# Kernel tuning notes

Hardware: AMD Instinct MI355X
Metric: run time of the kernel (lower is better)

## Reference

```python
import jax, jax.numpy as jnp
import numpy as np

B, LD, LQ = 32, 512, 32
E, NF = 300, 4
D = E + NF            # doc_input_size = 304
M = 16                # fofe_max_length == max_len
ALPHA = 0.9
VOCAB = 50000
H = 256
SAMPLE_NUM = 256
POS_N = 128           # int(sample_num * (1 - neg_ratio))
NEG_N = SAMPLE_NUM - POS_N
R = min(M, LD - 2)    # candidate negative lengths = 16
PPL = NEG_N // R + 1  # negatives drawn per length = 9


def setup_inputs() -> dict:
    key = jax.random.key(0)
    ks = jax.random.split(key, 16)
    emb = jax.random.normal(ks[0], (VOCAB, E), jnp.float32) * 0.1
    emb = emb.at[0].set(0.0)  # padding_idx=0
    doc = jax.random.randint(ks[1], (B, LD), 1, VOCAB)
    doc_f = jax.random.normal(ks[2], (B, LD, NF), jnp.float32) * 0.1
    query = jax.random.randint(ks[3], (B, LQ), 1, VOCAB)
    target_s = jax.random.randint(ks[4], (B,), 1, LD - M - 2)
    span = jax.random.randint(ks[5], (B,), 0, M)  # ans_span = target_e - target_s < fofe_max_length
    target_e = target_s + span
    rand_length = jax.random.permutation(ks[6], R)  # torch.randperm(min(max_len, L-2))
    # rand_position[i] ~ randint(1, LD - rand_length[i] - 1)
    u = jax.random.uniform(ks[7], (R, PPL))
    size = (LD - rand_length - 2).astype(jnp.float32)[:, None]
    rand_position = 1 + jnp.floor(u * size).astype(jnp.int32)
    rand_idx = jax.random.randint(ks[8], (NEG_N,), 0, B)  # faithful to original (dim-0 size used as bound)
    perm_idx = jax.random.permutation(ks[9], SAMPLE_NUM)

    def w(k, o, i):
        return jax.random.normal(k, (o, i), jnp.float32) * (1.0 / np.sqrt(i))

    CIN = 3 * D + E  # 1212
    W1 = w(ks[10], 4 * H, CIN)
    W2 = w(ks[11], 4 * H, 4 * H)
    W3 = w(ks[12], 4 * H, 4 * H)
    W4 = w(ks[13], 2 * H, 4 * H)
    W5 = w(ks[14], 1, 2 * H)
    doc_mask = jnp.zeros((B, LD), bool)
    query_mask = jnp.zeros((B, LQ), bool)
    return dict(doc=doc, doc_f=doc_f, query=query, target_s=target_s, target_e=target_e,
                doc_mask=doc_mask, query_mask=query_mask, emb=emb,
                W1=W1, W2=W2, W3=W3, W4=W4, W5=W5,
                rand_length=rand_length, rand_position=rand_position,
                rand_idx=rand_idx, perm_idx=perm_idx)


def _fofe_codes(x):
    """x: [B, D, LD] -> forward/inverse FOFE codes [B, D, M, LD].
    fwd[b,c,l,t] = sum_{k=0}^{l} alpha^k x[b,c,t-k]; inv mirrors to the right."""
    fwd_terms = jnp.stack(
        [(ALPHA ** k) * jnp.pad(x, ((0, 0), (0, 0), (k, 0)))[..., :LD] for k in range(M)], axis=2)
    inv_terms = jnp.stack(
        [(ALPHA ** k) * jnp.pad(x, ((0, 0), (0, 0), (0, k)))[..., k:] for k in range(M)], axis=2)
    return jnp.cumsum(fwd_terms, axis=2), jnp.cumsum(inv_terms, axis=2)


def _cnn(x, W1, W2, W3, W4, W5):
    h = jax.nn.relu(jnp.einsum('oi,bis->bos', W1, x))
    h = jax.nn.relu(jnp.einsum('oi,bis->bos', W2, h))
    h = jax.nn.relu(jnp.einsum('oi,bis->bos', W3, h))
    h = jax.nn.relu(jnp.einsum('oi,bis->bos', W4, h))
    return jax.nn.sigmoid(jnp.einsum('oi,bis->bos', W5, h))


def reference(doc, doc_f, query, target_s, target_e, doc_mask, query_mask, emb,
              W1, W2, W3, W4, W5, rand_length, rand_position, rand_idx, perm_idx):
    # input_embedding (dropout_emb = 0, pos/ner disabled)
    doc_input = jnp.concatenate([emb[doc], doc_f], axis=-1)  # [B, LD, D]
    x = jnp.swapaxes(doc_input, 1, 2)                         # [B, D, LD]
    fwd, inv = _fofe_codes(x)                                 # [B, D, M, LD] each

    # --- positive samples: gold span + left/right full contexts ---
    b = jnp.arange(B)
    span = target_e - target_s
    ans = fwd[b, :, span, target_e]                               # [B, D]
    l_ctx = fwd[b, :, M - 1, jnp.maximum(target_s - 1, 0)]        # [B, D]
    r_ctx = inv[b, :, M - 1, jnp.minimum(target_e + 1, LD - 1)]   # [B, D]
    pos = jnp.concatenate([l_ctx, ans, r_ctx], axis=-1)          # [B, 3D]
    pos = jnp.broadcast_to(pos[:, :, None], (B, 3 * D, POS_N))

    # --- negative samples: random spans of each length in rand_length ---
    rl = rand_length[:, None]                                     # [R, 1]
    neg_ans = fwd[:, :, rl, rand_position].reshape(B, D, R * PPL)
    neg_l = fwd[:, :, M - 1, rand_position - 1].reshape(B, D, R * PPL)
    neg_r = inv[:, :, M - 1, rand_position + rl + 1].reshape(B, D, R * PPL)
    rand_cat = jnp.concatenate([neg_l, neg_ans, neg_r], axis=1)   # [B, 3D, R*PPL]
    neg = rand_cat[:, :, rand_idx]                                # [B, 3D, NEG_N]

    # --- shuffle pos+neg, build query FOFE, run cnn, mse (sum) loss ---
    ctx_ans = jnp.concatenate([pos, neg], axis=-1)[:, :, perm_idx]
    target = jnp.concatenate(
        [jnp.ones((B, 1, POS_N), jnp.float32), jnp.zeros((B, 1, NEG_N), jnp.float32)],
        axis=-1)[:, :, perm_idx]
    qw = ALPHA ** jnp.arange(LQ - 1, -1, -1, dtype=jnp.float32)   # fofe_linear weights
    qf = jnp.einsum('t,bte->be', qw, emb[query])                  # [B, E]
    qb = jnp.broadcast_to(qf[:, :, None], (B, E, SAMPLE_NUM))
    dq_input = jnp.concatenate([ctx_ans, qb], axis=1)             # [B, 3D+E, S]
    score = _cnn(dq_input, W1, W2, W3, W4, W5)                    # [B, 1, S]
    loss = jnp.sum((score - target) ** 2)                         # mse_loss(size_average=False)
    return loss
```

## Files before the change

### kernel.cpp

```cpp
#include <hip/hip_runtime.h>
#include <hip/hip_bf16.h>

#define B_    32
#define LD_   512
#define LQ_   32
#define E_    300
#define NF_   4
#define D_    304
#define M_    16
#define ALPHA_ 0.9f
#define CIN_  1212
#define KP1_  1216
#define NCOL_ 1056
#define NPAD_ 1088
#define PPL_  9
#define NEG_N_ 128

typedef short short8 __attribute__((ext_vector_type(8)));
typedef float f32x4 __attribute__((ext_vector_type(4)));

__device__ __forceinline__ unsigned short f2bf(float f) {
    unsigned int x = __float_as_uint(f);
    unsigned int r = (x + 0x7FFFu + ((x >> 16) & 1u)) >> 16;
    return (unsigned short)r;
}
__device__ __forceinline__ float bf2f(unsigned short u) {
    return __uint_as_float(((unsigned int)u) << 16);
}

__global__ __launch_bounds__(128) void query_fofe(
    const int* __restrict__ query, const float* __restrict__ emb,
    unsigned short* __restrict__ qfb)
{
    int b = blockIdx.x;
    __shared__ int   rows[32];
    __shared__ float wq[32];
    int tid = threadIdx.x;
    if (tid < 32) {
        rows[tid] = query[b * LQ_ + tid];
        wq[tid] = powf(ALPHA_, (float)(LQ_ - 1 - tid));
    }
    __syncthreads();
    if (tid < 76) {
        int cc = tid * 4;
        float ax = 0.f, ay = 0.f, az = 0.f, aw = 0.f;
        if (cc < 300) {
            for (int i = 0; i < 32; ++i) {
                float4 v = *(const float4*)(emb + (size_t)rows[i] * E_ + cc);
                float wv = wq[i];
                ax += wv * v.x; ay += wv * v.y; az += wv * v.z; aw += wv * v.w;
            }
        }
        ushort4 o; o.x = f2bf(ax); o.y = f2bf(ay); o.z = f2bf(az); o.w = f2bf(aw);
        *(ushort4*)(qfb + (size_t)b * 304 + cc) = o;
    }
}

__global__ __launch_bounds__(320) void build_features(
    const int* __restrict__ doc, const float* __restrict__ doc_f,
    const int* __restrict__ target_s, const int* __restrict__ target_e,
    const float* __restrict__ emb,
    const int* __restrict__ rand_length, const int* __restrict__ rand_position,
    const unsigned short* __restrict__ qfb,
    unsigned short* __restrict__ Ft)
{
    int bcol = blockIdx.x;
    int b = bcol / 33;
    int col = bcol % 33;
    __shared__ int   s_t[3][16];
    __shared__ float s_w[3][16];
    __shared__ int   s_row[3][16];
    int tid = threadIdx.x;

    if (tid < 48) {
        int part = tid >> 4, k = tid & 15;
        int t; float valid;
        if (col == 0) {
            int ts = target_s[b], te = target_e[b];
            int span = te - ts;
            if (part == 0)      { t = ts - 1 - k;  valid = (t >= 0) ? 1.f : 0.f; }
            else if (part == 1) { t = te - k;      valid = (k <= span && t >= 0) ? 1.f : 0.f; }
            else                { t = te + 1 + k;  valid = (t < LD_) ? 1.f : 0.f; }
        } else {
            int j = col - 1;
            int r = j / PPL_, p = j - r * PPL_;
            int rl = rand_length[r];
            int rp = rand_position[r * PPL_ + p];
            if (part == 0)      { t = rp - 1 - k;      valid = (t >= 0) ? 1.f : 0.f; }
            else if (part == 1) { t = rp - k;          valid = (k <= rl && t >= 0) ? 1.f : 0.f; }
            else                { t = rp + rl + 1 + k; valid = (t < LD_) ? 1.f : 0.f; }
        }
        float w = (valid != 0.f) ? powf(ALPHA_, (float)k) : 0.f;
        t = min(max(t, 0), LD_ - 1);
        s_t[part][k] = t;
        s_w[part][k] = w;
        s_row[part][k] = doc[b * LD_ + t];
    }
    __syncthreads();

    unsigned short* out = Ft + (size_t)bcol * KP1_;
    int g = tid;
    if (g < 228) {
        int part = g / 76;
        int g2 = g - part * 76;
        int cc = g2 * 4;
        float ax = 0.f, ay = 0.f, az = 0.f, aw = 0.f;
        if (cc < 300) {
            for (int i = 0; i < 16; ++i) {
                float4 v = *(const float4*)(emb + (size_t)s_row[part][i] * E_ + cc);
                float wv = s_w[part][i];
                ax += wv * v.x; ay += wv * v.y; az += wv * v.z; aw += wv * v.w;
            }
        } else {
            for (int i = 0; i < 16; ++i) {
                float4 v = *(const float4*)(doc_f + ((size_t)b * LD_ + s_t[part][i]) * NF_);
                float wv = s_w[part][i];
                ax += wv * v.x; ay += wv * v.y; az += wv * v.z; aw += wv * v.w;
            }
        }
        ushort4 o; o.x = f2bf(ax); o.y = f2bf(ay); o.z = f2bf(az); o.w = f2bf(aw);
        *(ushort4*)(out + 4 * g) = o;
    } else if (g < 303) {
        *(ushort4*)(out + 4 * g) =
            *(const ushort4*)(qfb + (size_t)b * 304 + (g - 228) * 4);
    } else if (g == 303) {
        ushort4 z; z.x = 0; z.y = 0; z.z = 0; z.w = 0;
        *(ushort4*)(out + 4 * g) = z;
    }
}

__global__ __launch_bounds__(256) void convert_all(
    const float* __restrict__ W1, const float* __restrict__ W2,
    const float* __restrict__ W3, const float* __restrict__ W4,
    unsigned short* __restrict__ W1b, unsigned short* __restrict__ W2b,
    unsigned short* __restrict__ W3b, unsigned short* __restrict__ W4b)
{
    const long n1 = 1024L * KP1_ / 4;
    const long n2 = 1024L * 1024L / 4;
    const long n4 = 512L * 1024L / 4;
    const long total = n1 + 2 * n2 + n4;
    long stride = (long)gridDim.x * 256L;
    for (long i = (long)blockIdx.x * 256L + threadIdx.x; i < total; i += stride) {
        ushort4 o;
        if (i < n1) {
            long m = i / 304; int k4 = (int)(i - m * 304);
            if (k4 < 303) {
                float4 v = *(const float4*)(W1 + m * CIN_ + k4 * 4);
                o.x = f2bf(v.x); o.y = f2bf(v.y); o.z = f2bf(v.z); o.w = f2bf(v.w);
            } else { o.x = 0; o.y = 0; o.z = 0; o.w = 0; }
            *(ushort4*)(W1b + i * 4) = o;
        } else if (i < n1 + n2) {
            long j = i - n1;
            float4 v = *(const float4*)(W2 + j * 4);
            o.x = f2bf(v.x); o.y = f2bf(v.y); o.z = f2bf(v.z); o.w = f2bf(v.w);
            *(ushort4*)(W2b + j * 4) = o;
        } else if (i < n1 + 2 * n2) {
            long j = i - n1 - n2;
            float4 v = *(const float4*)(W3 + j * 4);
            o.x = f2bf(v.x); o.y = f2bf(v.y); o.z = f2bf(v.z); o.w = f2bf(v.w);
            *(ushort4*)(W3b + j * 4) = o;
        } else {
            long j = i - n1 - 2 * n2;
            float4 v = *(const float4*)(W4 + j * 4);
            o.x = f2bf(v.x); o.y = f2bf(v.y); o.z = f2bf(v.z); o.w = f2bf(v.w);
            *(ushort4*)(W4b + j * 4) = o;
        }
    }
}

__global__ __launch_bounds__(256) void gemm_relu(
    const unsigned short* __restrict__ A,
    const unsigned short* __restrict__ Bm,
    unsigned short* __restrict__ C,
    int M, int K)
{
    __shared__ unsigned short As[2][64][72];
    __shared__ unsigned short Bs[2][64][72];
    int tid = threadIdx.x;
    int m0 = blockIdx.x * 64, n0 = blockIdx.y * 64;
    int w = tid >> 6, lane = tid & 63;
    int wm = (w >> 1) * 32, wn = (w & 1) * 32;
    int lr = tid >> 2;
    int ls = (tid & 3) * 16;
    int fr = lane & 15, fk = (lane >> 4) * 8;

    const unsigned short* Arow = A + (size_t)(m0 + lr) * K + ls;
    const unsigned short* Brow = Bm + (size_t)(n0 + lr) * K + ls;

    f32x4 acc00 = {0.f,0.f,0.f,0.f}, acc01 = {0.f,0.f,0.f,0.f};
    f32x4 acc10 = {0.f,0.f,0.f,0.f}, acc11 = {0.f,0.f,0.f,0.f};

    int nk = K >> 6;
    {
        uint4 a0 = *(const uint4*)(Arow);
        uint4 a1 = *(const uint4*)(Arow + 8);
        uint4 b0 = *(const uint4*)(Brow);
        uint4 b1 = *(const uint4*)(Brow + 8);
        *(uint4*)&As[0][lr][ls]     = a0;
        *(uint4*)&As[0][lr][ls + 8] = a1;
        *(uint4*)&Bs[0][lr][ls]     = b0;
        *(uint4*)&Bs[0][lr][ls + 8] = b1;
    }
    __syncthreads();
    int cur = 0;
    for (int i = 0; i < nk; ++i) {
        uint4 na0, na1, nb0, nb1;
        bool more = (i + 1 < nk);
        if (more) {
            const unsigned short* An = Arow + (size_t)(i + 1) * 64;
            const unsigned short* Bn = Brow + (size_t)(i + 1) * 64;
            na0 = *(const uint4*)(An);
            na1 = *(const uint4*)(An + 8);
            nb0 = *(const uint4*)(Bn);
            nb1 = *(const uint4*)(Bn + 8);
        }
        #pragma unroll
        for (int s = 0; s < 2; ++s) {
            short8 fa0 = *(const short8*)&As[cur][wm + fr][s * 32 + fk];
            short8 fa1 = *(const short8*)&As[cur][wm + 16 + fr][s * 32 + fk];
            short8 fb0 = *(const short8*)&Bs[cur][wn + fr][s * 32 + fk];
            short8 fb1 = *(const short8*)&Bs[cur][wn + 16 + fr][s * 32 + fk];
            acc00 = __builtin_amdgcn_mfma_f32_16x16x32_bf16(fa0, fb0, acc00, 0, 0, 0);
            acc01 = __builtin_amdgcn_mfma_f32_16x16x32_bf16(fa0, fb1, acc01, 0, 0, 0);
            acc10 = __builtin_amdgcn_mfma_f32_16x16x32_bf16(fa1, fb0, acc10, 0, 0, 0);
            acc11 = __builtin_amdgcn_mfma_f32_16x16x32_bf16(fa1, fb1, acc11, 0, 0, 0);
        }
        if (more) {
            int nb = cur ^ 1;
            *(uint4*)&As[nb][lr][ls]     = na0;
            *(uint4*)&As[nb][lr][ls + 8] = na1;
            *(uint4*)&Bs[nb][lr][ls]     = nb0;
            *(uint4*)&Bs[nb][lr][ls + 8] = nb1;
        }
        __syncthreads();
        cur ^= 1;
    }

    int rbase = (lane >> 4) * 4;
    int cb = lane & 15;
    #define STORE_TILE(ACC, MT, NT) do {                                   \
        int m = m0 + wm + (MT) * 16 + rbase;                               \
        int n = n0 + wn + (NT) * 16 + cb;                                  \
        ushort4 o;                                                         \
        o.x = f2bf(fmaxf((ACC)[0], 0.f));                                  \
        o.y = f2bf(fmaxf((ACC)[1], 0.f));                                  \
        o.z = f2bf(fmaxf((ACC)[2], 0.f));                                  \
        o.w = f2bf(fmaxf((ACC)[3], 0.f));                                  \
        *(ushort4*)(C + (size_t)n * M + m) = o;                            \
    } while (0)
    STORE_TILE(acc00, 0, 0);
    STORE_TILE(acc01, 0, 1);
    STORE_TILE(acc10, 1, 0);
    STORE_TILE(acc11, 1, 1);
    #undef STORE_TILE
}

__global__ __launch_bounds__(256) void score_loss(
    const unsigned short* __restrict__ h4,
    const float* __restrict__ W5, const int* __restrict__ rand_idx,
    float* __restrict__ out)
{
    __shared__ int cnt[32];
    __shared__ float part[4];
    int tid = threadIdx.x;
    if (tid < 32) cnt[tid] = 0;
    __syncthreads();
    if (tid < NEG_N_) atomicAdd(&cnt[rand_idx[tid]], 1);
    __syncthreads();
    int w = tid >> 6, lane = tid & 63;
    int col = blockIdx.x * 4 + w;
    float v = 0.f;
    const unsigned short* row = h4 + (size_t)col * 512 + lane * 8;
    ushort4 v0 = *(const ushort4*)row;
    ushort4 v1 = *(const ushort4*)(row + 4);
    const float* w5 = W5 + lane * 8;
    float z = bf2f(v0.x) * w5[0] + bf2f(v0.y) * w5[1] +
              bf2f(v0.z) * w5[2] + bf2f(v0.w) * w5[3] +
              bf2f(v1.x) * w5[4] + bf2f(v1.y) * w5[5] +
              bf2f(v1.z) * w5[6] + bf2f(v1.w) * w5[7];
    for (int off = 32; off > 0; off >>= 1) z += __shfl_down(z, off, 64);
    if (lane == 0) {
        float s = 1.f / (1.f + expf(-z));
        int c33 = col % 33;
        if (c33 == 0) { float d = s - 1.f; v = 128.f * d * d; }
        else          { v = (float)cnt[c33 - 1] * s * s; }
        part[w] = v;
    }
    __syncthreads();
    if (tid == 0) atomicAdd(out, part[0] + part[1] + part[2] + part[3]);
}

extern "C" void kernel_launch(void* const* d_in, const int* in_sizes, int n_in,
                              void* d_out, int out_size, void* d_ws, size_t ws_size,
                              hipStream_t stream)
{
    const int*   doc        = (const int*)d_in[0];
    const float* doc_f      = (const float*)d_in[1];
    const int*   query      = (const int*)d_in[2];
    const int*   target_s   = (const int*)d_in[3];
    const int*   target_e   = (const int*)d_in[4];
    const float* emb        = (const float*)d_in[7];
    const float* W1         = (const float*)d_in[8];
    const float* W2         = (const float*)d_in[9];
    const float* W3         = (const float*)d_in[10];
    const float* W4         = (const float*)d_in[11];
    const float* W5         = (const float*)d_in[12];
    const int*   rand_length   = (const int*)d_in[13];
    const int*   rand_position = (const int*)d_in[14];
    const int*   rand_idx      = (const int*)d_in[15];

    char* ws = (char*)d_ws;
    size_t off = 0;
    auto alloc = [&](size_t bytes) {
        void* p = ws + off;
        off = (off + bytes + 255) & ~(size_t)255;
        return p;
    };
    unsigned short* W1b = (unsigned short*)alloc((size_t)1024 * KP1_ * 2);
    unsigned short* W2b = (unsigned short*)alloc((size_t)1024 * 1024 * 2);
    unsigned short* W3b = (unsigned short*)alloc((size_t)1024 * 1024 * 2);
    unsigned short* W4b = (unsigned short*)alloc((size_t)512 * 1024 * 2);
    unsigned short* Ft  = (unsigned short*)alloc((size_t)NPAD_ * KP1_ * 2);
    unsigned short* hA  = (unsigned short*)alloc((size_t)NPAD_ * 1024 * 2);
    unsigned short* hB  = (unsigned short*)alloc((size_t)NPAD_ * 1024 * 2);
    unsigned short* qfb = (unsigned short*)alloc((size_t)B_ * 304 * 2);
    float* d_loss = (float*)d_out;
    (void)ws_size; (void)in_sizes; (void)n_in; (void)out_size;

    hipMemsetAsync(Ft + (size_t)NCOL_ * KP1_, 0,
                   (size_t)(NPAD_ - NCOL_) * KP1_ * 2, stream);
    hipMemsetAsync(d_loss, 0, sizeof(float), stream);

    convert_all<<<dim3(3776), dim3(256), 0, stream>>>(W1, W2, W3, W4,
                                                      W1b, W2b, W3b, W4b);
    query_fofe<<<dim3(B_), dim3(128), 0, stream>>>(query, emb, qfb);
    build_features<<<dim3(NCOL_), dim3(320), 0, stream>>>(
        doc, doc_f, target_s, target_e, emb,
        rand_length, rand_position, qfb, Ft);

    gemm_relu<<<dim3(16, 17), dim3(256), 0, stream>>>(W1b, Ft, hA, 1024, KP1_);
    gemm_relu<<<dim3(16, 17), dim3(256), 0, stream>>>(W2b, hA, hB, 1024, 1024);
    gemm_relu<<<dim3(16, 17), dim3(256), 0, stream>>>(W3b, hB, hA, 1024, 1024);
    gemm_relu<<<dim3(8, 17),  dim3(256), 0, stream>>>(W4b, hA, hB, 512, 1024);

    score_loss<<<dim3(NCOL_ / 4), dim3(256), 0, stream>>>(hB, W5, rand_idx, d_loss);
}
```

Before: 195.1 us.

## Fuse prep kernels, split-K GEMM with 128-wide K tiles, fuse final layer into score

Merges query FOFE, feature building, weight conversion and padding/zero fills into a single prep launch, dropping the memsets and separate kernels; query FOFE is now recomputed per column block. The GEMM is rewritten so each of four waves handles a 32-slice of a 128-wide K tile and covers the full 64x64 output, with partial sums reduced through LDS; K for layer 1 is padded to 1280. The last GEMM folds ReLU and the W5 dot product into its epilogue, accumulating scores via atomics, and a single-block kernel computes the loss. This cuts launches and removes the h4 round trip, at the cost of losing double buffering, adding an LDS reduction, and redundant query work.

```diff
diff --git a/kernel.cpp b/kernel.cpp
--- a/kernel.cpp
+++ b/kernel.cpp
@@ -10,7 +10,7 @@
 #define M_    16
 #define ALPHA_ 0.9f
 #define CIN_  1212
-#define KP1_  1216
+#define KP1_  1280
 #define NCOL_ 1056
 #define NPAD_ 1088
 #define PPL_  9
@@ -28,266 +28,286 @@
     return __uint_as_float(((unsigned int)u) << 16);
 }
 
-__global__ __launch_bounds__(128) void query_fofe(
-    const int* __restrict__ query, const float* __restrict__ emb,
-    unsigned short* __restrict__ qfb)
-{
-    int b = blockIdx.x;
-    __shared__ int   rows[32];
-    __shared__ float wq[32];
-    int tid = threadIdx.x;
-    if (tid < 32) {
-        rows[tid] = query[b * LQ_ + tid];
-        wq[tid] = powf(ALPHA_, (float)(LQ_ - 1 - tid));
-    }
-    __syncthreads();
-    if (tid < 76) {
-        int cc = tid * 4;
-        float ax = 0.f, ay = 0.f, az = 0.f, aw = 0.f;
-        if (cc < 300) {
-            for (int i = 0; i < 32; ++i) {
-                float4 v = *(const float4*)(emb + (size_t)rows[i] * E_ + cc);
-                float wv = wq[i];
-                ax += wv * v.x; ay += wv * v.y; az += wv * v.z; aw += wv * v.w;
-            }
-        }
-        ushort4 o; o.x = f2bf(ax); o.y = f2bf(ay); o.z = f2bf(az); o.w = f2bf(aw);
-        *(ushort4*)(qfb + (size_t)b * 304 + cc) = o;
-    }
-}
-
-__global__ __launch_bounds__(320) void build_features(
+__global__ __launch_bounds__(320) void prep(
     const int* __restrict__ doc, const float* __restrict__ doc_f,
+    const int* __restrict__ query,
     const int* __restrict__ target_s, const int* __restrict__ target_e,
     const float* __restrict__ emb,
     const int* __restrict__ rand_length, const int* __restrict__ rand_position,
-    const unsigned short* __restrict__ qfb,
-    unsigned short* __restrict__ Ft)
-{
-    int bcol = blockIdx.x;
-    int b = bcol / 33;
-    int col = bcol % 33;
-    __shared__ int   s_t[3][16];
-    __shared__ float s_w[3][16];
-    __shared__ int   s_row[3][16];
-    int tid = threadIdx.x;
-
-    if (tid < 48) {
-        int part = tid >> 4, k = tid & 15;
-        int t; float valid;
-        if (col == 0) {
-            int ts = target_s[b], te = target_e[b];
-            int span = te - ts;
-            if (part == 0)      { t = ts - 1 - k;  valid = (t >= 0) ? 1.f : 0.f; }
-            else if (part == 1) { t = te - k;      valid = (k <= span && t >= 0) ? 1.f : 0.f; }
-            else                { t = te + 1 + k;  valid = (t < LD_) ? 1.f : 0.f; }
-        } else {
-            int j = col - 1;
-            int r = j / PPL_, p = j - r * PPL_;
-            int rl = rand_length[r];
-            int rp = rand_position[r * PPL_ + p];
-            if (part == 0)      { t = rp - 1 - k;      valid = (t >= 0) ? 1.f : 0.f; }
-            else if (part == 1) { t = rp - k;          valid = (k <= rl && t >= 0) ? 1.f : 0.f; }
-            else                { t = rp + rl + 1 + k; valid = (t < LD_) ? 1.f : 0.f; }
-        }
-        float w = (valid != 0.f) ? powf(ALPHA_, (float)k) : 0.f;
-        t = min(max(t, 0), LD_ - 1);
-        s_t[part][k] = t;
-        s_w[part][k] = w;
-        s_row[part][k] = doc[b * LD_ + t];
-    }
-    __syncthreads();
-
-    unsigned short* out = Ft + (size_t)bcol * KP1_;
-    int g = tid;
-    if (g < 228) {
-        int part = g / 76;
-        int g2 = g - part * 76;
-        int cc = g2 * 4;
-        float ax = 0.f, ay = 0.f, az = 0.f, aw = 0.f;
-        if (cc < 300) {
-            for (int i = 0; i < 16; ++i) {
-                float4 v = *(const float4*)(emb + (size_t)s_row[part][i] * E_ + cc);
-                float wv = s_w[part][i];
-                ax += wv * v.x; ay += wv * v.y; az += wv * v.z; aw += wv * v.w;
-            }
-        } else {
-            for (int i = 0; i < 16; ++i) {
-                float4 v = *(const float4*)(doc_f + ((size_t)b * LD_ + s_t[part][i]) * NF_);
-                float wv = s_w[part][i];
-                ax += wv * v.x; ay += wv * v.y; az += wv * v.z; aw += wv * v.w;
-            }
-        }
-        ushort4 o; o.x = f2bf(ax); o.y = f2bf(ay); o.z = f2bf(az); o.w = f2bf(aw);
-        *(ushort4*)(out + 4 * g) = o;
-    } else if (g < 303) {
-        *(ushort4*)(out + 4 * g) =
-            *(const ushort4*)(qfb + (size_t)b * 304 + (g - 228) * 4);
-    } else if (g == 303) {
-        ushort4 z; z.x = 0; z.y = 0; z.z = 0; z.w = 0;
-        *(ushort4*)(out + 4 * g) = z;
-    }
-}
-
-__global__ __launch_bounds__(256) void convert_all(
     const float* __restrict__ W1, const float* __restrict__ W2,
     const float* __restrict__ W3, const float* __restrict__ W4,
     unsigned short* __restrict__ W1b, unsigned short* __restrict__ W2b,
-    unsigned short* __restrict__ W3b, unsigned short* __restrict__ W4b)
-{
-    const long n1 = 1024L * KP1_ / 4;
-    const long n2 = 1024L * 1024L / 4;
-    const long n4 = 512L * 1024L / 4;
-    const long total = n1 + 2 * n2 + n4;
-    long stride = (long)gridDim.x * 256L;
-    for (long i = (long)blockIdx.x * 256L + threadIdx.x; i < total; i += stride) {
-        ushort4 o;
-        if (i < n1) {
-            long m = i / 304; int k4 = (int)(i - m * 304);
-            if (k4 < 303) {
-                float4 v = *(const float4*)(W1 + m * CIN_ + k4 * 4);
+    unsigned short* __restrict__ W3b, unsigned short* __restrict__ W4b,
+    unsigned short* __restrict__ Ft, float* __restrict__ zbuf)
+{
+    int bid = blockIdx.x;
+    int tid = threadIdx.x;
+
+    if (bid < NCOL_) {
+        int b = bid / 33;
+        int col = bid % 33;
+        __shared__ int   s_t[3][16];
+        __shared__ float s_w[3][16];
+        __shared__ int   s_row[3][16];
+        if (tid < 48) {
+            int part = tid >> 4, k = tid & 15;
+            int t; float valid;
+            if (col == 0) {
+                int ts = target_s[b], te = target_e[b];
+                int span = te - ts;
+                if (part == 0)      { t = ts - 1 - k;  valid = (t >= 0) ? 1.f : 0.f; }
+                else if (part == 1) { t = te - k;      valid = (k <= span && t >= 0) ? 1.f : 0.f; }
+                else                { t = te + 1 + k;  valid = (t < LD_) ? 1.f : 0.f; }
+            } else {
+                int j = col - 1;
+                int r = j / PPL_, p = j - r * PPL_;
+                int rl = rand_length[r];
+                int rp = rand_position[r * PPL_ + p];
+                if (part == 0)      { t = rp - 1 - k;      valid = (t >= 0) ? 1.f : 0.f; }
+                else if (part == 1) { t = rp - k;          valid = (k <= rl && t >= 0) ? 1.f : 0.f; }
+                else                { t = rp + rl + 1 + k; valid = (t < LD_) ? 1.f : 0.f; }
+            }
+            float w = (valid != 0.f) ? powf(ALPHA_, (float)k) : 0.f;
+            t = min(max(t, 0), LD_ - 1);
+            s_t[part][k] = t;
+            s_w[part][k] = w;
+            s_row[part][k] = doc[b * LD_ + t];
+        }
+        __syncthreads();
+
+        unsigned short* out = Ft + (size_t)bid * KP1_;
+        int g = tid;
+        if (g < 228) {
+            int part = g / 76;
+            int g2 = g - part * 76;
+            int cc = g2 * 4;
+            float ax = 0.f, ay = 0.f, az = 0.f, aw = 0.f;
+            if (cc < 300) {
+                for (int i = 0; i < 16; ++i) {
+                    float4 v = *(const float4*)(emb + (size_t)s_row[part][i] * E_ + cc);
+                    float wv = s_w[part][i];
+                    ax += wv * v.x; ay += wv * v.y; az += wv * v.z; aw += wv * v.w;
+                }
+            } else {
+                for (int i = 0; i < 16; ++i) {
+                    float4 v = *(const float4*)(doc_f + ((size_t)b * LD_ + s_t[part][i]) * NF_);
+                    float wv = s_w[part][i];
+                    ax += wv * v.x; ay += wv * v.y; az += wv * v.z; aw += wv * v.w;
+                }
+            }
+            ushort4 o; o.x = f2bf(ax); o.y = f2bf(ay); o.z = f2bf(az); o.w = f2bf(aw);
+            *(ushort4*)(out + 4 * g) = o;
+        } else if (g < 303) {
+            int ce = (g - 228) * 4;
+            float ax = 0.f, ay = 0.f, az = 0.f, aw = 0.f;
+            float wv = powf(ALPHA_, (float)(LQ_ - 1));
+            for (int i = 0; i < 32; ++i) {
+                int row = query[b * LQ_ + i];
+                float4 v = *(const float4*)(emb + (size_t)row * E_ + ce);
+                ax += wv * v.x; ay += wv * v.y; az += wv * v.z; aw += wv * v.w;
+                wv *= (1.0f / ALPHA_);
+            }
+            ushort4 o; o.x = f2bf(ax); o.y = f2bf(ay); o.z = f2bf(az); o.w = f2bf(aw);
+            *(ushort4*)(out + 4 * g) = o;
+        } else {
+            ushort4 z; z.x = 0; z.y = 0; z.z = 0; z.w = 0;
+            *(ushort4*)(out + 4 * g) = z;
+        }
+    } else if (bid < 2000) {
+        const long n1 = 1024L * (KP1_ / 4);
+        const long n2 = 1024L * 1024L / 4;
+        const long n4 = 512L * 1024L / 4;
+        const long total = n1 + 2 * n2 + n4;
+        long stride = 944L * 320L;
+        for (long i = (long)(bid - NCOL_) * 320L + tid; i < total; i += stride) {
+            ushort4 o;
+            if (i < n1) {
+                long m = i / 320; int k4 = (int)(i - m * 320);
+                if (k4 < 303) {
+                    float4 v = *(const float4*)(W1 + m * CIN_ + k4 * 4);
+                    o.x = f2bf(v.x); o.y = f2bf(v.y); o.z = f2bf(v.z); o.w = f2bf(v.w);
+                } else { o.x = 0; o.y = 0; o.z = 0; o.w = 0; }
+                *(ushort4*)(W1b + i * 4) = o;
+            } else if (i < n1 + n2) {
+                long j = i - n1;
+                float4 v = *(const float4*)(W2 + j * 4);
                 o.x = f2bf(v.x); o.y = f2bf(v.y); o.z = f2bf(v.z); o.w = f2bf(v.w);
-            } else { o.x = 0; o.y = 0; o.z = 0; o.w = 0; }
-            *(ushort4*)(W1b + i * 4) = o;
-        } else if (i < n1 + n2) {
-            long j = i - n1;
-            float4 v = *(const float4*)(W2 + j * 4);
-            o.x = f2bf(v.x); o.y = f2bf(v.y); o.z = f2bf(v.z); o.w = f2bf(v.w);
-            *(ushort4*)(W2b + j * 4) = o;
-        } else if (i < n1 + 2 * n2) {
-            long j = i - n1 - n2;
-            float4 v = *(const float4*)(W3 + j * 4);
-            o.x = f2bf(v.x); o.y = f2bf(v.y); o.z = f2bf(v.z); o.w = f2bf(v.w);
-            *(ushort4*)(W3b + j * 4) = o;
-        } else {
-            long j = i - n1 - 2 * n2;
-            float4 v = *(const float4*)(W4 + j * 4);
-            o.x = f2bf(v.x); o.y = f2bf(v.y); o.z = f2bf(v.z); o.w = f2bf(v.w);
-            *(ushort4*)(W4b + j * 4) = o;
-        }
-    }
-}
+                *(ushort4*)(W2b + j * 4) = o;
+            } else if (i < n1 + 2 * n2) {
+                long j = i - n1 - n2;
+                float4 v = *(const float4*)(W3 + j * 4);
+                o.x = f2bf(v.x); o.y = f2bf(v.y); o.z = f2bf(v.z); o.w = f2bf(v.w);
+                *(ushort4*)(W3b + j * 4) = o;
+            } else {
+                long j = i - n1 - 2 * n2;
+                float4 v = *(const float4*)(W4 + j * 4);
+                o.x = f2bf(v.x); o.y = f2bf(v.y); o.z = f2bf(v.z); o.w = f2bf(v.w);
+                *(ushort4*)(W4b + j * 4) = o;
+            }
+        }
+    } else if (bid < 2032) {
+        int row = NCOL_ + (bid - 2000);
+        ushort4 z; z.x = 0; z.y = 0; z.z = 0; z.w = 0;
+        *(ushort4*)(Ft + (size_t)row * KP1_ + tid * 4) = z;
+    } else {
+        for (int i = tid; i < NPAD_; i += 320) zbuf[i] = 0.f;
+    }
+}
+
+#define GEMM_CORE(A_, B_PTR_, M_ARG_, K_ARG_)                                 \
+    int tid = threadIdx.x, lane = tid & 63, w = tid >> 6;                     \
+    int m0 = blockIdx.x * 64, n0 = blockIdx.y * 64;                           \
+    int fr = lane & 15, fq = lane >> 4, fk = fq * 8, kw = w * 32;             \
+    int ar = tid >> 2, ac = (tid & 3) * 32;                                   \
+    const unsigned short* Ag = (A_) + (size_t)(m0 + ar) * (K_ARG_) + ac;      \
+    const unsigned short* Bg = (B_PTR_) + (size_t)(n0 + ar) * (K_ARG_) + ac;  \
+    f32x4 acc[16];                                                            \
+    _Pragma("unroll")                                                         \
+    for (int t = 0; t < 16; ++t) { acc[t][0]=0.f; acc[t][1]=0.f; acc[t][2]=0.f; acc[t][3]=0.f; } \
+    int nk = (K_ARG_) >> 7;                                                   \
+    uint4 pa0, pa1, pa2, pa3, pb0, pb1, pb2, pb3;                             \
+    pa0 = *(const uint4*)(Ag);      pa1 = *(const uint4*)(Ag + 8);            \
+    pa2 = *(const uint4*)(Ag + 16); pa3 = *(const uint4*)(Ag + 24);           \
+    pb0 = *(const uint4*)(Bg);      pb1 = *(const uint4*)(Bg + 8);            \
+    pb2 = *(const uint4*)(Bg + 16); pb3 = *(const uint4*)(Bg + 24);           \
+    for (int i = 0; i < nk; ++i) {                                            \
+        *(uint4*)&sh.s.A[ar][ac]      = pa0;                                  \
+        *(uint4*)&sh.s.A[ar][ac + 8]  = pa1;                                  \
+        *(uint4*)&sh.s.A[ar][ac + 16] = pa2;                                  \
+        *(uint4*)&sh.s.A[ar][ac + 24] = pa3;                                  \
+        *(uint4*)&sh.s.B[ar][ac]      = pb0;                                  \
+        *(uint4*)&sh.s.B[ar][ac + 8]  = pb1;                                  \
+        *(uint4*)&sh.s.B[ar][ac + 16] = pb2;                                  \
+        *(uint4*)&sh.s.B[ar][ac + 24] = pb3;                                  \
+        __syncthreads();                                                      \
+        if (i + 1 < nk) {                                                     \
+            const unsigned short* An = Ag + (size_t)(i + 1) * 128;            \
+            const unsigned short* Bn = Bg + (size_t)(i + 1) * 128;            \
+            pa0 = *(const uint4*)(An);      pa1 = *(const uint4*)(An + 8);    \
+            pa2 = *(const uint4*)(An + 16); pa3 = *(const uint4*)(An + 24);   \
+            pb0 = *(const uint4*)(Bn);      pb1 = *(const uint4*)(Bn + 8);    \
+            pb2 = *(const uint4*)(Bn + 16); pb3 = *(const uint4*)(Bn + 24);   \
+        }                                                                     \
+        short8 af[4], bfr[4];                                                 \
+        _Pragma("unroll")                                                     \
+        for (int mt = 0; mt < 4; ++mt)                                        \
+            af[mt] = *(const short8*)&sh.s.A[mt * 16 + fr][kw + fk];          \
+        _Pragma("unroll")                                                     \
+        for (int nt = 0; nt < 4; ++nt)                                        \
+            bfr[nt] = *(const short8*)&sh.s.B[nt * 16 + fr][kw + fk];         \
+        _Pragma("unroll")                                                     \
+        for (int mt = 0; mt < 4; ++mt)                                        \
+            _Pragma("unroll")                                                 \
+            for (int nt = 0; nt < 4; ++nt)                                    \
+                acc[mt * 4 + nt] = __builtin_amdgcn_mfma_f32_16x16x32_bf16(   \
+                    af[mt], bfr[nt], acc[mt * 4 + nt], 0, 0, 0);              \
+        __syncthreads();                                                      \
+    }                                                                         \
+     \
+    if (w == 1 || w == 3) {                                                   \
+        int r = w >> 1;                                                       \
+        _Pragma("unroll")                                                     \
+        for (int t = 0; t < 16; ++t) *(f32x4*)&sh.red[r][t][lane][0] = acc[t];\
+    }                                                                         \
+    __syncthreads();                                                          \
+    if (w == 0 || w == 2) {                                                   \
+        int r = w >> 1;                                                       \
+        _Pragma("unroll")                                                     \
+        for (int t = 0; t < 16; ++t) {                                        \
+            f32x4 v = *(const f32x4*)&sh.red[r][t][lane][0];                  \
+            acc[t][0]+=v[0]; acc[t][1]+=v[1]; acc[t][2]+=v[2]; acc[t][3]+=v[3]; \
+        }                                                                     \
+    }                                                                         \
+    __syncthreads();                                                          \
+    if (w == 2) {                                                             \
+        _Pragma("unroll")                                                     \
+        for (int t = 0; t < 16; ++t) *(f32x4*)&sh.red[0][t][lane][0] = acc[t];\
+    }                                                                         \
+    __syncthreads();
+
+union GemmLds {
+    struct { unsigned short A[64][136]; unsigned short B[64][136]; } s;
+    float red[2][16][64][4];
+};
 
 __global__ __launch_bounds__(256) void gemm_relu(
     const unsigned short* __restrict__ A,
     const unsigned short* __restrict__ Bm,
-    unsigned short* __restrict__ C,
-    int M, int K)
-{
-    __shared__ unsigned short As[2][64][72];
-    __shared__ unsigned short Bs[2][64][72];
-    int tid = threadIdx.x;
-    int m0 = blockIdx.x * 64, n0 = blockIdx.y * 64;
-    int w = tid >> 6, lane = tid & 63;
-    int wm = (w >> 1) * 32, wn = (w & 1) * 32;
-    int lr = tid >> 2;
-    int ls = (tid & 3) * 16;
-    int fr = lane & 15, fk = (lane >> 4) * 8;
-
-    const unsigned short* Arow = A + (size_t)(m0 + lr) * K + ls;
-    const unsigned short* Brow = Bm + (size_t)(n0 + lr) * K + ls;
-
-    f32x4 acc00 = {0.f,0.f,0.f,0.f}, acc01 = {0.f,0.f,0.f,0.f};
-    f32x4 acc10 = {0.f,0.f,0.f,0.f}, acc11 = {0.f,0.f,0.f,0.f};
-
-    int nk = K >> 6;
-    {
-        uint4 a0 = *(const uint4*)(Arow);
-        uint4 a1 = *(const uint4*)(Arow + 8);
-        uint4 b0 = *(const uint4*)(Brow);
-        uint4 b1 = *(const uint4*)(Brow + 8);
-        *(uint4*)&As[0][lr][ls]     = a0;
-        *(uint4*)&As[0][lr][ls + 8] = a1;
-        *(uint4*)&Bs[0][lr][ls]     = b0;
-        *(uint4*)&Bs[0][lr][ls + 8] = b1;
-    }
-    __syncthreads();
-    int cur = 0;
-    for (int i = 0; i < nk; ++i) {
-        uint4 na0, na1, nb0, nb1;
-        bool more = (i + 1 < nk);
-        if (more) {
-            const unsigned short* An = Arow + (size_t)(i + 1) * 64;
-            const unsigned short* Bn = Brow + (size_t)(i + 1) * 64;
-            na0 = *(const uint4*)(An);
-            na1 = *(const uint4*)(An + 8);
-            nb0 = *(const uint4*)(Bn);
-            nb1 = *(const uint4*)(Bn + 8);
-        }
+    unsigned short* __restrict__ C, int M, int K)
+{
+    __shared__ GemmLds sh;
+    GEMM_CORE(A, Bm, M, K)
+    if (w == 0) {
         #pragma unroll
-        for (int s = 0; s < 2; ++s) {
-            short8 fa0 = *(const short8*)&As[cur][wm + fr][s * 32 + fk];
-            short8 fa1 = *(const short8*)&As[cur][wm + 16 + fr][s * 32 + fk];
-            short8 fb0 = *(const short8*)&Bs[cur][wn + fr][s * 32 + fk];
-            short8 fb1 = *(const short8*)&Bs[cur][wn + 16 + fr][s * 32 + fk];
-            acc00 = __builtin_amdgcn_mfma_f32_16x16x32_bf16(fa0, fb0, acc00, 0, 0, 0);
-            acc01 = __builtin_amdgcn_mfma_f32_16x16x32_bf16(fa0, fb1, acc01, 0, 0, 0);
-            acc10 = __builtin_amdgcn_mfma_f32_16x16x32_bf16(fa1, fb0, acc10, 0, 0, 0);
-            acc11 = __builtin_amdgcn_mfma_f32_16x16x32_bf16(fa1, fb1, acc11, 0, 0, 0);
-        }
-        if (more) {
-            int nb = cur ^ 1;
-            *(uint4*)&As[nb][lr][ls]     = na0;
-            *(uint4*)&As[nb][lr][ls + 8] = na1;
-            *(uint4*)&Bs[nb][lr][ls]     = nb0;
-            *(uint4*)&Bs[nb][lr][ls + 8] = nb1;
-        }
-        __syncthreads();
-        cur ^= 1;
-    }
-
-    int rbase = (lane >> 4) * 4;
-    int cb = lane & 15;
-    #define STORE_TILE(ACC, MT, NT) do {                                   \
-        int m = m0 + wm + (MT) * 16 + rbase;                               \
-        int n = n0 + wn + (NT) * 16 + cb;                                  \
-        ushort4 o;                                                         \
-        o.x = f2bf(fmaxf((ACC)[0], 0.f));                                  \
-        o.y = f2bf(fmaxf((ACC)[1], 0.f));                                  \
-        o.z = f2bf(fmaxf((ACC)[2], 0.f));                                  \
-        o.w = f2bf(fmaxf((ACC)[3], 0.f));                                  \
-        *(ushort4*)(C + (size_t)n * M + m) = o;                            \
-    } while (0)
-    STORE_TILE(acc00, 0, 0);
-    STORE_TILE(acc01, 0, 1);
-    STORE_TILE(acc10, 1, 0);
-    STORE_TILE(acc11, 1, 1);
-    #undef STORE_TILE
-}
-
-__global__ __launch_bounds__(256) void score_loss(
-    const unsigned short* __restrict__ h4,
-    const float* __restrict__ W5, const int* __restrict__ rand_idx,
+        for (int t = 0; t < 16; ++t) {
+            f32x4 v = *(const f32x4*)&sh.red[0][t][lane][0];
+            f32x4 s = acc[t];
+            s[0]+=v[0]; s[1]+=v[1]; s[2]+=v[2]; s[3]+=v[3];
+            int m = m0 + (t >> 2) * 16 + fq * 4;
+            int n = n0 + (t & 3) * 16 + fr;
+            ushort4 o;
+            o.x = f2bf(fmaxf(s[0], 0.f));
+            o.y = f2bf(fmaxf(s[1], 0.f));
+            o.z = f2bf(fmaxf(s[2], 0.f));
+            o.w = f2bf(fmaxf(s[3], 0.f));
+            *(ushort4*)(C + (size_t)n * M + m) = o;
+        }
+    }
+}
+
+__global__ __launch_bounds__(256) void gemm4_score(
+    const unsigned short* __restrict__ A,
+    const unsigned short* __restrict__ Bm,
+    const float* __restrict__ W5, float* __restrict__ zbuf, int M, int K)
+{
+    __shared__ GemmLds sh;
+    GEMM_CORE(A, Bm, M, K)
+    if (w == 0) {
+        #pragma unroll
+        for (int t = 0; t < 16; ++t) {
+            f32x4 v = *(const f32x4*)&sh.red[0][t][lane][0];
+            f32x4 s = acc[t];
+            s[0]+=v[0]; s[1]+=v[1]; s[2]+=v[2]; s[3]+=v[3];
+            int m = m0 + (t >> 2) * 16 + fq * 4;
+            float p = fmaxf(s[0], 0.f) * W5[m]
+                    + fmaxf(s[1], 0.f) * W5[m + 1]
+                    + fmaxf(s[2], 0.f) * W5[m + 2]
+                    + fmaxf(s[3], 0.f) * W5[m + 3];
+            p += __shfl_down(p, 32);
+            p += __shfl_down(p, 16);
+            if (fq == 0) {
+                int n = n0 + (t & 3) * 16 + fr;
+                atomicAdd(&zbuf[n], p);
+            }
+        }
+    }
+}
+
+__global__ __launch_bounds__(256) void loss_k(
+    const float* __restrict__ zbuf, const int* __restrict__ rand_idx,
     float* __restrict__ out)
 {
     __shared__ int cnt[32];
-    __shared__ float part[4];
+    __shared__ float red[256];
     int tid = threadIdx.x;
     if (tid < 32) cnt[tid] = 0;
     __syncthreads();
     if (tid < NEG_N_) atomicAdd(&cnt[rand_idx[tid]], 1);
     __syncthreads();
-    int w = tid >> 6, lane = tid & 63;
-    int col = blockIdx.x * 4 + w;
-    float v = 0.f;
-    const unsigned short* row = h4 + (size_t)col * 512 + lane * 8;
-    ushort4 v0 = *(const ushort4*)row;
-    ushort4 v1 = *(const ushort4*)(row + 4);
-    const float* w5 = W5 + lane * 8;
-    float z = bf2f(v0.x) * w5[0] + bf2f(v0.y) * w5[1] +
-              bf2f(v0.z) * w5[2] + bf2f(v0.w) * w5[3] +
-              bf2f(v1.x) * w5[4] + bf2f(v1.y) * w5[5] +
-              bf2f(v1.z) * w5[6] + bf2f(v1.w) * w5[7];
-    for (int off = 32; off > 0; off >>= 1) z += __shfl_down(z, off, 64);
-    if (lane == 0) {
-        float s = 1.f / (1.f + expf(-z));
-        int c33 = col % 33;
-        if (c33 == 0) { float d = s - 1.f; v = 128.f * d * d; }
-        else          { v = (float)cnt[c33 - 1] * s * s; }
-        part[w] = v;
-    }
+    float acc = 0.f;
+    for (int c = tid; c < NCOL_; c += 256) {
+        float s = 1.f / (1.f + expf(-zbuf[c]));
+        int c33 = c % 33;
+        if (c33 == 0) { float d = s - 1.f; acc += 128.f * d * d; }
+        else          { acc += (float)cnt[c33 - 1] * s * s; }
+    }
+    red[tid] = acc;
     __syncthreads();
-    if (tid == 0) atomicAdd(out, part[0] + part[1] + part[2] + part[3]);
+    for (int off = 128; off > 0; off >>= 1) {
+        if (tid < off) red[tid] += red[tid + off];
+        __syncthreads();
+    }
+    if (tid == 0) out[0] = red[0];
 }
 
 extern "C" void kernel_launch(void* const* d_in, const int* in_sizes, int n_in,
@@ -323,25 +343,19 @@
     unsigned short* Ft  = (unsigned short*)alloc((size_t)NPAD_ * KP1_ * 2);
     unsigned short* hA  = (unsigned short*)alloc((size_t)NPAD_ * 1024 * 2);
     unsigned short* hB  = (unsigned short*)alloc((size_t)NPAD_ * 1024 * 2);
-    unsigned short* qfb = (unsigned short*)alloc((size_t)B_ * 304 * 2);
+    float* zbuf         = (float*)alloc((size_t)NPAD_ * sizeof(float));
     float* d_loss = (float*)d_out;
     (void)ws_size; (void)in_sizes; (void)n_in; (void)out_size;
 
-    hipMemsetAsync(Ft + (size_t)NCOL_ * KP1_, 0,
-                   (size_t)(NPAD_ - NCOL_) * KP1_ * 2, stream);
-    hipMemsetAsync(d_loss, 0, sizeof(float), stream);
-
-    convert_all<<<dim3(3776), dim3(256), 0, stream>>>(W1, W2, W3, W4,
-                                                      W1b, W2b, W3b, W4b);
-    query_fofe<<<dim3(B_), dim3(128), 0, stream>>>(query, emb, qfb);
-    build_features<<<dim3(NCOL_), dim3(320), 0, stream>>>(
-        doc, doc_f, target_s, target_e, emb,
-        rand_length, rand_position, qfb, Ft);
+    prep<<<dim3(2033), dim3(320), 0, stream>>>(
+        doc, doc_f, query, target_s, target_e, emb,
+        rand_length, rand_position,
+        W1, W2, W3, W4, W1b, W2b, W3b, W4b, Ft, zbuf);
 
     gemm_relu<<<dim3(16, 17), dim3(256), 0, stream>>>(W1b, Ft, hA, 1024, KP1_);
     gemm_relu<<<dim3(16, 17), dim3(256), 0, stream>>>(W2b, hA, hB, 1024, 1024);
     gemm_relu<<<dim3(16, 17), dim3(256), 0, stream>>>(W3b, hB, hA, 1024, 1024);
-    gemm_relu<<<dim3(8, 17),  dim3(256), 0, stream>>>(W4b, hA, hB, 512, 1024);
-
-    score_loss<<<dim3(NCOL_ / 4), dim3(256), 0, stream>>>(hB, W5, rand_idx, d_loss);
-}
+    gemm4_score<<<dim3(8, 17), dim3(256), 0, stream>>>(W4b, hA, W5, zbuf, 512, 1024);
+
+    loss_k<<<dim3(1), dim3(256), 0, stream>>>(zbuf, rand_idx, d_loss);
+}
```

New measurement: 226.0 us. +15.8%, slower.
